# Performance work log

Hardware: AMD Instinct MI355X
Metric: run time of the kernel (lower is better)

## Reference

```python
import jax, jax.numpy as jnp
import numpy as np

N = 2_097_152   # total nodes
G = 8_192       # graphs in the batch
T = 1_000       # diffusion steps


def setup_inputs() -> dict:
    key = jax.random.key(0)
    k1, k2, k3, k4, k5 = jax.random.split(key, 5)
    x0 = jax.random.normal(k1, (N, 3), jnp.float32)
    x1 = jax.random.normal(k2, (N, 3), jnp.float32)
    noise = jax.random.normal(k3, (N, 3), jnp.float32)
    beta = jnp.linspace(1e-4, 0.02, T).astype(jnp.float32)
    batch = jnp.sort(jax.random.randint(k4, (N,), 0, G, jnp.int32))
    time = jax.random.randint(k5, (N,), 0, T, jnp.int32)
    return dict(x0=x0, x1=x1, noise=noise, beta=beta, batch=batch, time=time)


def reference(x0, x1, noise, beta, batch, time):
    # ---- schedule buffers (computed from beta exactly as in __init__) ----
    std_fwd = jnp.sqrt(jnp.cumsum(beta))                      # [T]
    std_bwd = jnp.sqrt(jnp.flip(jnp.cumsum(jnp.flip(beta))))  # [T]
    denom = std_bwd ** 2 + std_fwd ** 2
    mu_x0 = std_fwd ** 2 / denom   # coef1 with sigma1=std_bwd, sigma2=std_fwd
    mu_x1 = std_bwd ** 2 / denom
    std_sb = jnp.sqrt(std_bwd ** 2 * std_fwd ** 2 / denom)

    # extract(coef, time, dim)[batch] == coef[time][batch] (per-node gather)
    idx = time[batch]                                         # [N]
    x_t = (mu_x0[idx, None] * x0 + mu_x1[idx, None] * x1
           + std_sb[idx, None] * noise)                       # [N,3]

    # ---- fused unbatch + match_com + Kabsch align over all G graphs ----
    seg = lambda v: jax.ops.segment_sum(v, batch, num_segments=G,
                                        indices_are_sorted=True)
    cnt = jnp.maximum(seg(jnp.ones((N,), x0.dtype)), 1.0)[:, None]  # [G,1]
    com_x0 = seg(x0) / cnt                                    # [G,3]
    com_xt = seg(x_t) / cnt                                   # [G,3]
    x0c = x0 - com_x0[batch]   # match_com: shift x0 COM onto x_t COM
    xtc = x_t - com_xt[batch]

    # Kabsch: H_g = sum_i x0c_i xtc_i^T  -> rotation mapping x0 onto x_t
    H = seg(x0c[:, :, None] * xtc[:, None, :])                # [G,3,3]
    U, S, Vt = jnp.linalg.svd(H)
    d = jnp.sign(jnp.linalg.det(U) * jnp.linalg.det(Vt))      # [G]
    D = jnp.stack([jnp.ones_like(d), jnp.ones_like(d), d], axis=-1)  # [G,3]
    # R = V diag(1,1,d) U^T,  R_ij = Vt_ki D_k U_jk
    R = jnp.einsum('gki,gk,gjk->gij', Vt, D, U)               # [G,3,3]

    aligned_x0 = jnp.einsum('nij,nj->ni', R[batch], x0c) + com_xt[batch]

    target = (x_t - aligned_x0) / std_fwd[idx, None]
    return x_t, target
```

## Files before the change

kernel.cpp:

```cpp
#include <hip/hip_runtime.h>
#include <math.h>

#define GMAX 8192

__device__ float g_sched[4 * 1024];
__device__ int   g_starts[GMAX + 1];
__device__ float g_gparams[GMAX * 16];

__global__ __launch_bounds__(1024) void k_sched(const float* __restrict__ beta, int T) {
    __shared__ double sbeta[1024];
    __shared__ double buf[2][1024];
    int t = threadIdx.x;
    double b = (t < T) ? (double)beta[t] : 0.0;
    sbeta[t] = b;
    buf[0][t] = b;
    __syncthreads();
    int src = 0;
    for (int off = 1; off < 1024; off <<= 1) {
        double v = buf[src][t];
        if (t >= off) v += buf[src][t - off];
        buf[src ^ 1][t] = v;
        src ^= 1;
        __syncthreads();
    }
    double total = buf[src][T - 1];
    if (t < T) {
        double fwd2 = buf[src][t];
        double bwd2 = total - fwd2 + sbeta[t];
        double denom = fwd2 + bwd2;
        g_sched[t]          = (float)(fwd2 / denom);
        g_sched[1024 + t]   = (float)(bwd2 / denom);
        g_sched[2048 + t]   = (float)sqrt(fwd2 * bwd2 / denom);
        g_sched[3072 + t]   = (float)(1.0 / sqrt(fwd2));
    }
}

__global__ void k_starts(const int* __restrict__ batch, int N, int G) {
    int g = blockIdx.x * blockDim.x + threadIdx.x;
    if (g > G) return;
    int lo = 0, hi = N;
    while (lo < hi) {
        int mid = (lo + hi) >> 1;
        if (batch[mid] < g) lo = mid + 1; else hi = mid;
    }
    g_starts[g] = lo;
}

__device__ void kabsch_store(const float* sum, int n, float c0, float c1,
                             float cs, float isf, float* p) {
    double fn = (double)(n > 0 ? n : 1);
    double H[3][3];
    #pragma unroll
    for (int a = 0; a < 3; ++a)
        #pragma unroll
        for (int b = 0; b < 3; ++b)
            H[a][b] = (double)sum[6 + 3*a + b] - (double)sum[a] * (double)sum[3 + b] / fn;

    double A[3][3];
    #pragma unroll
    for (int i = 0; i < 3; ++i)
        #pragma unroll
        for (int j = 0; j < 3; ++j) {
            double acc = 0.0;
            #pragma unroll
            for (int k = 0; k < 3; ++k) acc += H[k][i] * H[k][j];
            A[i][j] = acc;
        }

    double V[3][3] = {{1,0,0},{0,1,0},{0,0,1}};
    for (int sweep = 0; sweep < 20; ++sweep) {
        double off = A[0][1]*A[0][1] + A[0][2]*A[0][2] + A[1][2]*A[1][2];
        double diag = A[0][0]*A[0][0] + A[1][1]*A[1][1] + A[2][2]*A[2][2];
        if (off <= 1e-28 * (diag + 1e-300)) break;
        for (int pi = 0; pi < 3; ++pi) {
            int P = (pi == 0) ? 0 : (pi == 1) ? 0 : 1;
            int Q = (pi == 0) ? 1 : (pi == 1) ? 2 : 2;
            double apq = A[P][Q];
            if (apq == 0.0) continue;
            double theta = (A[Q][Q] - A[P][P]) / (2.0 * apq);
            double tt = ((theta >= 0.0) ? 1.0 : -1.0) /
                        (fabs(theta) + sqrt(theta * theta + 1.0));
            double c = 1.0 / sqrt(tt * tt + 1.0);
            double s = tt * c;
            double app = A[P][P], aqq = A[Q][Q];
            A[P][P] = app - tt * apq;
            A[Q][Q] = aqq + tt * apq;
            A[P][Q] = A[Q][P] = 0.0;
            int Rr = 3 - P - Q;
            double arp = A[Rr][P], arq = A[Rr][Q];
            A[Rr][P] = A[P][Rr] = c * arp - s * arq;
            A[Rr][Q] = A[Q][Rr] = s * arp + c * arq;
            #pragma unroll
            for (int i = 0; i < 3; ++i) {
                double vip = V[i][P], viq = V[i][Q];
                V[i][P] = c * vip - s * viq;
                V[i][Q] = s * vip + c * viq;
            }
        }
    }
    double w[3] = {A[0][0], A[1][1], A[2][2]};
    int o0 = 0, o1 = 1, o2 = 2, tmp;
    if (w[o0] < w[o1]) { tmp = o0; o0 = o1; o1 = tmp; }
    if (w[o0] < w[o2]) { tmp = o0; o0 = o2; o2 = tmp; }
    if (w[o1] < w[o2]) { tmp = o1; o1 = o2; o2 = tmp; }

    double s0 = sqrt(fmax(w[o0], 0.0));
    double s1 = sqrt(fmax(w[o1], 0.0));
    double s2 = sqrt(fmax(w[o2], 0.0));
    double det = H[0][0]*(H[1][1]*H[2][2] - H[1][2]*H[2][1])
               - H[0][1]*(H[1][0]*H[2][2] - H[1][2]*H[2][0])
               + H[0][2]*(H[1][0]*H[2][1] - H[1][1]*H[2][0]);
    double d = (det >= 0.0) ? 1.0 : -1.0;
    double thr = 1e-9 * s0;
    double i0 = (s0 > 1e-300) ? 1.0 / s0 : 0.0;
    double i1 = (s1 > thr) ? 1.0 / s1 : 0.0;
    double i2 = (s2 > thr) ? d / s2 : 0.0;

    double B[3][3];
    #pragma unroll
    for (int i = 0; i < 3; ++i)
        #pragma unroll
        for (int j = 0; j < 3; ++j)
            B[i][j] = V[i][o0] * i0 * V[j][o0]
                    + V[i][o1] * i1 * V[j][o1]
                    + V[i][o2] * i2 * V[j][o2];

    double Rm[3][3];
    #pragma unroll
    for (int i = 0; i < 3; ++i)
        #pragma unroll
        for (int j = 0; j < 3; ++j)
            Rm[i][j] = B[i][0]*H[j][0] + B[i][1]*H[j][1] + B[i][2]*H[j][2];

    double com0[3], comt[3];
    #pragma unroll
    for (int a = 0; a < 3; ++a) { com0[a] = sum[a] / fn; comt[a] = sum[3+a] / fn; }

    #pragma unroll
    for (int i = 0; i < 3; ++i)
        #pragma unroll
        for (int j = 0; j < 3; ++j)
            p[3*i + j] = (float)Rm[i][j];
    #pragma unroll
    for (int i = 0; i < 3; ++i)
        p[9 + i] = (float)(comt[i] - (Rm[i][0]*com0[0] + Rm[i][1]*com0[1] + Rm[i][2]*com0[2]));
    p[12] = c0; p[13] = c1; p[14] = cs; p[15] = isf;
}

__global__ __launch_bounds__(256) void k_reduce(const float* __restrict__ x0,
                                               const float* __restrict__ x1,
                                               const float* __restrict__ noise,
                                               const int* __restrict__ tarr,
                                               float* __restrict__ out_xt) {
    int g = blockIdx.x;
    int s = g_starts[g], e = g_starts[g + 1];
    int tg = tarr[g];
    float c0 = g_sched[tg];
    float c1 = g_sched[1024 + tg];
    float cs = g_sched[2048 + tg];
    float isf = g_sched[3072 + tg];

    float acc[15];
    #pragma unroll
    for (int k = 0; k < 15; ++k) acc[k] = 0.0f;

    for (int i = s + (int)threadIdx.x; i < e; i += 256) {
        float a0 = x0[3*i], a1 = x0[3*i+1], a2 = x0[3*i+2];
        float b0 = x1[3*i], b1 = x1[3*i+1], b2 = x1[3*i+2];
        float n0 = noise[3*i], n1 = noise[3*i+1], n2 = noise[3*i+2];
        float t0 = c0*a0 + c1*b0 + cs*n0;
        float t1 = c0*a1 + c1*b1 + cs*n1;
        float t2 = c0*a2 + c1*b2 + cs*n2;
        out_xt[3*i] = t0; out_xt[3*i+1] = t1; out_xt[3*i+2] = t2;
        acc[0] += a0; acc[1] += a1; acc[2] += a2;
        acc[3] += t0; acc[4] += t1; acc[5] += t2;
        acc[6]  += a0*t0; acc[7]  += a0*t1; acc[8]  += a0*t2;
        acc[9]  += a1*t0; acc[10] += a1*t1; acc[11] += a1*t2;
        acc[12] += a2*t0; acc[13] += a2*t1; acc[14] += a2*t2;
    }

    #pragma unroll
    for (int k = 0; k < 15; ++k) {
        #pragma unroll
        for (int off = 32; off > 0; off >>= 1)
            acc[k] += __shfl_down(acc[k], off, 64);
    }
    __shared__ float red[4][15];
    int wid = threadIdx.x >> 6, lane = threadIdx.x & 63;
    if (lane == 0) {
        #pragma unroll
        for (int k = 0; k < 15; ++k) red[wid][k] = acc[k];
    }
    __syncthreads();
    if (threadIdx.x == 0) {
        float sum[15];
        #pragma unroll
        for (int k = 0; k < 15; ++k)
            sum[k] = red[0][k] + red[1][k] + red[2][k] + red[3][k];
        kabsch_store(sum, e - s, c0, c1, cs, isf, &g_gparams[g * 16]);
    }
}

__global__ __launch_bounds__(256) void k_final(const float* __restrict__ x0,
                                              const int* __restrict__ batch,
                                              const float* __restrict__ xt,
                                              float* __restrict__ out_tg,
                                              int N) {
    int i = blockIdx.x * 256 + (int)threadIdx.x;
    if (i >= N) return;
    int g = batch[i];
    const float* p = &g_gparams[g * 16];
    float a0 = x0[3*i], a1 = x0[3*i+1], a2 = x0[3*i+2];
    float t0 = xt[3*i], t1 = xt[3*i+1], t2 = xt[3*i+2];
    float al0 = p[0]*a0 + p[1]*a1 + p[2]*a2 + p[9];
    float al1 = p[3]*a0 + p[4]*a1 + p[5]*a2 + p[10];
    float al2 = p[6]*a0 + p[7]*a1 + p[8]*a2 + p[11];
    float isf = p[15];
    out_tg[3*i]   = (t0 - al0) * isf;
    out_tg[3*i+1] = (t1 - al1) * isf;
    out_tg[3*i+2] = (t2 - al2) * isf;
}

extern "C" void kernel_launch(void* const* d_in, const int* in_sizes, int n_in,
                              void* d_out, int out_size, void* d_ws, size_t ws_size,
                              hipStream_t stream) {
    const float* x0    = (const float*)d_in[0];
    const float* x1    = (const float*)d_in[1];
    const float* noise = (const float*)d_in[2];
    const float* beta  = (const float*)d_in[3];
    const int*   batch = (const int*)d_in[4];
    const int*   tarr  = (const int*)d_in[5];

    int N = in_sizes[4];
    int T = in_sizes[3];
    int G = GMAX;

    float* out_xt = (float*)d_out;
    float* out_tg = out_xt + (size_t)3 * N;

    k_sched<<<1, 1024, 0, stream>>>(beta, T);
    k_starts<<<(G + 1 + 255) / 256, 256, 0, stream>>>(batch, N, G);
    k_reduce<<<G, 256, 0, stream>>>(x0, x1, noise, tarr, out_xt);
    k_final<<<(N + 255) / 256, 256, 0, stream>>>(x0, batch, out_xt, out_tg, N);
}
```

Before: 196.7 us.

## Stage node data via float4 shared loads and split Kabsch into its own kernel

Merges the schedule and segment-start kernels into one launch. The reduce and final kernels now load x0, x1, noise and xt as float4 into shared memory per 256-node chunk, instead of doing strided scalar loads of 3-float records. The serial double-precision Kabsch solve, which ran on thread 0 at the end of every reduce block, moves to a separate kernel with one thread per graph, and per-graph sums pass through a global buffer. The final kernel runs one block per graph, so it no longer reads `batch`. The costs are an extra launch, extra `__syncthreads` per chunk, and idle lanes in partial chunks.

Measured after the change: 175.0 us. 1.12x faster.

```diff
diff --git a/kernel.cpp b/kernel.cpp
--- a/kernel.cpp
+++ b/kernel.cpp
@@ -5,45 +5,49 @@
 
 __device__ float g_sched[4 * 1024];
 __device__ int   g_starts[GMAX + 1];
+__device__ float g_sums[GMAX * 16];
 __device__ float g_gparams[GMAX * 16];
 
-__global__ __launch_bounds__(1024) void k_sched(const float* __restrict__ beta, int T) {
-    __shared__ double sbeta[1024];
-    __shared__ double buf[2][1024];
-    int t = threadIdx.x;
-    double b = (t < T) ? (double)beta[t] : 0.0;
-    sbeta[t] = b;
-    buf[0][t] = b;
-    __syncthreads();
-    int src = 0;
-    for (int off = 1; off < 1024; off <<= 1) {
-        double v = buf[src][t];
-        if (t >= off) v += buf[src][t - off];
-        buf[src ^ 1][t] = v;
-        src ^= 1;
-        __syncthreads();
-    }
-    double total = buf[src][T - 1];
-    if (t < T) {
-        double fwd2 = buf[src][t];
-        double bwd2 = total - fwd2 + sbeta[t];
-        double denom = fwd2 + bwd2;
-        g_sched[t]          = (float)(fwd2 / denom);
-        g_sched[1024 + t]   = (float)(bwd2 / denom);
-        g_sched[2048 + t]   = (float)sqrt(fwd2 * bwd2 / denom);
-        g_sched[3072 + t]   = (float)(1.0 / sqrt(fwd2));
-    }
-}
-
-__global__ void k_starts(const int* __restrict__ batch, int N, int G) {
-    int g = blockIdx.x * blockDim.x + threadIdx.x;
-    if (g > G) return;
-    int lo = 0, hi = N;
-    while (lo < hi) {
-        int mid = (lo + hi) >> 1;
-        if (batch[mid] < g) lo = mid + 1; else hi = mid;
-    }
-    g_starts[g] = lo;
+__global__ __launch_bounds__(1024) void k_prep(const float* __restrict__ beta,
+                                               const int* __restrict__ batch,
+                                               int T, int N, int G) {
+    if (blockIdx.x == 0) {
+        __shared__ double sbeta[1024];
+        __shared__ double buf[2][1024];
+        int t = threadIdx.x;
+        double b = (t < T) ? (double)beta[t] : 0.0;
+        sbeta[t] = b;
+        buf[0][t] = b;
+        __syncthreads();
+        int src = 0;
+        for (int off = 1; off < 1024; off <<= 1) {
+            double v = buf[src][t];
+            if (t >= off) v += buf[src][t - off];
+            buf[src ^ 1][t] = v;
+            src ^= 1;
+            __syncthreads();
+        }
+        double total = buf[src][T - 1];
+        if (t < T) {
+            double fwd2 = buf[src][t];
+            double bwd2 = total - fwd2 + sbeta[t];
+            double denom = fwd2 + bwd2;
+            g_sched[t]        = (float)(fwd2 / denom);
+            g_sched[1024 + t] = (float)(bwd2 / denom);
+            g_sched[2048 + t] = (float)sqrt(fwd2 * bwd2 / denom);
+            g_sched[3072 + t] = (float)(1.0 / sqrt(fwd2));
+        }
+    } else {
+        int g = (int)(blockIdx.x - 1) * 1024 + (int)threadIdx.x;
+        if (g <= G) {
+            int lo = 0, hi = N;
+            while (lo < hi) {
+                int mid = (lo + hi) >> 1;
+                if (batch[mid] < g) lo = mid + 1; else hi = mid;
+            }
+            g_starts[g] = lo;
+        }
+    }
 }
 
 __device__ void kabsch_store(const float* sum, int n, float c0, float c1,
@@ -82,9 +86,9 @@
                         (fabs(theta) + sqrt(theta * theta + 1.0));
             double c = 1.0 / sqrt(tt * tt + 1.0);
             double s = tt * c;
-            double app = A[P][P], aqq = A[Q][Q];
-            A[P][P] = app - tt * apq;
-            A[Q][Q] = aqq + tt * apq;
+            double apq2 = A[P][Q];
+            A[P][P] -= tt * apq2;
+            A[Q][Q] += tt * apq2;
             A[P][Q] = A[Q][P] = 0.0;
             int Rr = 3 - P - Q;
             double arp = A[Rr][P], arq = A[Rr][Q];
@@ -148,77 +152,139 @@
 }
 
 __global__ __launch_bounds__(256) void k_reduce(const float* __restrict__ x0,
-                                               const float* __restrict__ x1,
-                                               const float* __restrict__ noise,
-                                               const int* __restrict__ tarr,
-                                               float* __restrict__ out_xt) {
+                                                const float* __restrict__ x1,
+                                                const float* __restrict__ noise,
+                                                const int* __restrict__ tarr,
+                                                float* __restrict__ out_xt,
+                                                int total4) {
+    __shared__ __align__(16) float sA[776];
+    __shared__ __align__(16) float sB[776];
+    __shared__ __align__(16) float sN[776];
+    __shared__ float red[15][257];
+
     int g = blockIdx.x;
     int s = g_starts[g], e = g_starts[g + 1];
     int tg = tarr[g];
     float c0 = g_sched[tg];
     float c1 = g_sched[1024 + tg];
     float cs = g_sched[2048 + tg];
+
+    float acc[15];
+    #pragma unroll
+    for (int k = 0; k < 15; ++k) acc[k] = 0.0f;
+
+    const int tid = (int)threadIdx.x;
+
+    for (int cb = s; cb < e; cb += 256) {
+        int m = e - cb; if (m > 256) m = 256;
+        int fb = (3 * cb) & ~3;
+        int nf4 = ((3 * (cb + m)) - fb + 3) >> 2;
+        if (tid < nf4) {
+            int i4 = (fb >> 2) + tid;
+            if (i4 < total4) {
+                ((float4*)sA)[tid] = ((const float4*)x0)[i4];
+                ((float4*)sB)[tid] = ((const float4*)x1)[i4];
+                ((float4*)sN)[tid] = ((const float4*)noise)[i4];
+            }
+        }
+        __syncthreads();
+        if (tid < m) {
+            int off = 3 * (cb + tid) - fb;
+            float a0 = sA[off], a1 = sA[off+1], a2 = sA[off+2];
+            float b0 = sB[off], b1 = sB[off+1], b2 = sB[off+2];
+            float n0 = sN[off], n1 = sN[off+1], n2 = sN[off+2];
+            float t0 = c0*a0 + c1*b0 + cs*n0;
+            float t1 = c0*a1 + c1*b1 + cs*n1;
+            float t2 = c0*a2 + c1*b2 + cs*n2;
+            int oi = 3 * (cb + tid);
+            out_xt[oi] = t0; out_xt[oi+1] = t1; out_xt[oi+2] = t2;
+            acc[0] += a0; acc[1] += a1; acc[2] += a2;
+            acc[3] += t0; acc[4] += t1; acc[5] += t2;
+            acc[6]  += a0*t0; acc[7]  += a0*t1; acc[8]  += a0*t2;
+            acc[9]  += a1*t0; acc[10] += a1*t1; acc[11] += a1*t2;
+            acc[12] += a2*t0; acc[13] += a2*t1; acc[14] += a2*t2;
+        }
+        __syncthreads();
+    }
+
+    #pragma unroll
+    for (int v = 0; v < 15; ++v) red[v][tid] = acc[v];
+    __syncthreads();
+    int wv = tid >> 6;
+    int lane = tid & 63;
+    int v = wv * 4 + (lane >> 4);
+    int sub = lane & 15;
+    float x = 0.0f;
+    if (v < 15) {
+        #pragma unroll
+        for (int k = 0; k < 16; ++k) x += red[v][sub + (k << 4)];
+    }
+    x += __shfl_down(x, 8, 64);
+    x += __shfl_down(x, 4, 64);
+    x += __shfl_down(x, 2, 64);
+    x += __shfl_down(x, 1, 64);
+    if (v < 15 && sub == 0) g_sums[g * 16 + v] = x;
+}
+
+__global__ __launch_bounds__(256) void k_kabsch(const int* __restrict__ tarr) {
+    int g = blockIdx.x * 256 + (int)threadIdx.x;
+    if (g >= GMAX) return;
+    float sum[15];
+    #pragma unroll
+    for (int k = 0; k < 15; ++k) sum[k] = g_sums[g * 16 + k];
+    int n = g_starts[g + 1] - g_starts[g];
+    int tg = tarr[g];
+    float c0 = g_sched[tg];
+    float c1 = g_sched[1024 + tg];
+    float cs = g_sched[2048 + tg];
     float isf = g_sched[3072 + tg];
-
-    float acc[15];
-    #pragma unroll
-    for (int k = 0; k < 15; ++k) acc[k] = 0.0f;
-
-    for (int i = s + (int)threadIdx.x; i < e; i += 256) {
-        float a0 = x0[3*i], a1 = x0[3*i+1], a2 = x0[3*i+2];
-        float b0 = x1[3*i], b1 = x1[3*i+1], b2 = x1[3*i+2];
-        float n0 = noise[3*i], n1 = noise[3*i+1], n2 = noise[3*i+2];
-        float t0 = c0*a0 + c1*b0 + cs*n0;
-        float t1 = c0*a1 + c1*b1 + cs*n1;
-        float t2 = c0*a2 + c1*b2 + cs*n2;
-        out_xt[3*i] = t0; out_xt[3*i+1] = t1; out_xt[3*i+2] = t2;
-        acc[0] += a0; acc[1] += a1; acc[2] += a2;
-        acc[3] += t0; acc[4] += t1; acc[5] += t2;
-        acc[6]  += a0*t0; acc[7]  += a0*t1; acc[8]  += a0*t2;
-        acc[9]  += a1*t0; acc[10] += a1*t1; acc[11] += a1*t2;
-        acc[12] += a2*t0; acc[13] += a2*t1; acc[14] += a2*t2;
-    }
-
-    #pragma unroll
-    for (int k = 0; k < 15; ++k) {
-        #pragma unroll
-        for (int off = 32; off > 0; off >>= 1)
-            acc[k] += __shfl_down(acc[k], off, 64);
-    }
-    __shared__ float red[4][15];
-    int wid = threadIdx.x >> 6, lane = threadIdx.x & 63;
-    if (lane == 0) {
-        #pragma unroll
-        for (int k = 0; k < 15; ++k) red[wid][k] = acc[k];
-    }
-    __syncthreads();
-    if (threadIdx.x == 0) {
-        float sum[15];
-        #pragma unroll
-        for (int k = 0; k < 15; ++k)
-            sum[k] = red[0][k] + red[1][k] + red[2][k] + red[3][k];
-        kabsch_store(sum, e - s, c0, c1, cs, isf, &g_gparams[g * 16]);
-    }
+    kabsch_store(sum, n, c0, c1, cs, isf, &g_gparams[g * 16]);
 }
 
 __global__ __launch_bounds__(256) void k_final(const float* __restrict__ x0,
-                                              const int* __restrict__ batch,
-                                              const float* __restrict__ xt,
-                                              float* __restrict__ out_tg,
-                                              int N) {
-    int i = blockIdx.x * 256 + (int)threadIdx.x;
-    if (i >= N) return;
-    int g = batch[i];
+                                               const float* __restrict__ xt,
+                                               float* __restrict__ out_tg,
+                                               int total4) {
+    __shared__ __align__(16) float sA[776];
+    __shared__ __align__(16) float sT[776];
+    int g = blockIdx.x;
+    int s = g_starts[g], e = g_starts[g + 1];
+    if (s >= e) return;
+
     const float* p = &g_gparams[g * 16];
-    float a0 = x0[3*i], a1 = x0[3*i+1], a2 = x0[3*i+2];
-    float t0 = xt[3*i], t1 = xt[3*i+1], t2 = xt[3*i+2];
-    float al0 = p[0]*a0 + p[1]*a1 + p[2]*a2 + p[9];
-    float al1 = p[3]*a0 + p[4]*a1 + p[5]*a2 + p[10];
-    float al2 = p[6]*a0 + p[7]*a1 + p[8]*a2 + p[11];
+    float r00 = p[0], r01 = p[1], r02 = p[2];
+    float r10 = p[3], r11 = p[4], r12 = p[5];
+    float r20 = p[6], r21 = p[7], r22 = p[8];
+    float tv0 = p[9], tv1 = p[10], tv2 = p[11];
     float isf = p[15];
-    out_tg[3*i]   = (t0 - al0) * isf;
-    out_tg[3*i+1] = (t1 - al1) * isf;
-    out_tg[3*i+2] = (t2 - al2) * isf;
+
+    const int tid = (int)threadIdx.x;
+    for (int cb = s; cb < e; cb += 256) {
+        int m = e - cb; if (m > 256) m = 256;
+        int fb = (3 * cb) & ~3;
+        int nf4 = ((3 * (cb + m)) - fb + 3) >> 2;
+        if (tid < nf4) {
+            int i4 = (fb >> 2) + tid;
+            if (i4 < total4) {
+                ((float4*)sA)[tid] = ((const float4*)x0)[i4];
+                ((float4*)sT)[tid] = ((const float4*)xt)[i4];
+            }
+        }
+        __syncthreads();
+        if (tid < m) {
+            int off = 3 * (cb + tid) - fb;
+            float a0 = sA[off], a1 = sA[off+1], a2 = sA[off+2];
+            float w0 = sT[off], w1 = sT[off+1], w2 = sT[off+2];
+            float al0 = r00*a0 + r01*a1 + r02*a2 + tv0;
+            float al1 = r10*a0 + r11*a1 + r12*a2 + tv1;
+            float al2 = r20*a0 + r21*a1 + r22*a2 + tv2;
+            int oi = 3 * (cb + tid);
+            out_tg[oi]   = (w0 - al0) * isf;
+            out_tg[oi+1] = (w1 - al1) * isf;
+            out_tg[oi+2] = (w2 - al2) * isf;
+        }
+        __syncthreads();
+    }
 }
 
 extern "C" void kernel_launch(void* const* d_in, const int* in_sizes, int n_in,
@@ -234,12 +300,13 @@
     int N = in_sizes[4];
     int T = in_sizes[3];
     int G = GMAX;
+    int total4 = (3 * N) >> 2;
 
     float* out_xt = (float*)d_out;
     float* out_tg = out_xt + (size_t)3 * N;
 
-    k_sched<<<1, 1024, 0, stream>>>(beta, T);
-    k_starts<<<(G + 1 + 255) / 256, 256, 0, stream>>>(batch, N, G);
-    k_reduce<<<G, 256, 0, stream>>>(x0, x1, noise, tarr, out_xt);
-    k_final<<<(N + 255) / 256, 256, 0, stream>>>(x0, batch, out_xt, out_tg, N);
-}
+    k_prep<<<1 + (G + 1 + 1023) / 1024, 1024, 0, stream>>>(beta, batch, T, N, G);
+    k_reduce<<<G, 256, 0, stream>>>(x0, x1, noise, tarr, out_xt, total4);
+    k_kabsch<<<(G + 255) / 256, 256, 0, stream>>>(tarr);
+    k_final<<<G, 256, 0, stream>>>(x0, out_xt, out_tg, total4);
+}
```

## Replace per-graph reduction with flat node-parallel segmented reduction and atomics

Applied to the files above, without the earlier changes.

Per-graph blocks with binary-searched segment starts are replaced by a flat kernel in which each thread handles four nodes through float4 loads. Each wavefront does a segmented shuffle reduction and flushes per-graph sums, including the node count, to a global buffer with atomics. The Kabsch solve moves to its own one-thread-per-graph kernel, and the final pass is vectorised the same way. This targets the load imbalance and uncoalesced stride-3 accesses of the block-per-graph reduction, at the cost of atomic contention, float atomic nondeterminism, and the assumption that N is a multiple of 1024.

Result: faster. 168.3 us (-14.4%).

```diff
diff --git a/kernel.cpp b/kernel.cpp
--- a/kernel.cpp
+++ b/kernel.cpp
@@ -4,46 +4,117 @@
 #define GMAX 8192
 
 __device__ float g_sched[4 * 1024];
-__device__ int   g_starts[GMAX + 1];
+__device__ float g_sums[GMAX * 16];
 __device__ float g_gparams[GMAX * 16];
 
-__global__ __launch_bounds__(1024) void k_sched(const float* __restrict__ beta, int T) {
-    __shared__ double sbeta[1024];
-    __shared__ double buf[2][1024];
-    int t = threadIdx.x;
-    double b = (t < T) ? (double)beta[t] : 0.0;
-    sbeta[t] = b;
-    buf[0][t] = b;
-    __syncthreads();
-    int src = 0;
-    for (int off = 1; off < 1024; off <<= 1) {
-        double v = buf[src][t];
-        if (t >= off) v += buf[src][t - off];
-        buf[src ^ 1][t] = v;
-        src ^= 1;
+__global__ __launch_bounds__(1024) void k_prep(const float* __restrict__ beta, int T) {
+    if (blockIdx.x == 0) {
+        __shared__ double sbeta[1024];
+        __shared__ double buf[2][1024];
+        int t = threadIdx.x;
+        double b = (t < T) ? (double)beta[t] : 0.0;
+        sbeta[t] = b;
+        buf[0][t] = b;
         __syncthreads();
-    }
-    double total = buf[src][T - 1];
-    if (t < T) {
-        double fwd2 = buf[src][t];
-        double bwd2 = total - fwd2 + sbeta[t];
-        double denom = fwd2 + bwd2;
-        g_sched[t]          = (float)(fwd2 / denom);
-        g_sched[1024 + t]   = (float)(bwd2 / denom);
-        g_sched[2048 + t]   = (float)sqrt(fwd2 * bwd2 / denom);
-        g_sched[3072 + t]   = (float)(1.0 / sqrt(fwd2));
-    }
-}
-
-__global__ void k_starts(const int* __restrict__ batch, int N, int G) {
-    int g = blockIdx.x * blockDim.x + threadIdx.x;
-    if (g > G) return;
-    int lo = 0, hi = N;
-    while (lo < hi) {
-        int mid = (lo + hi) >> 1;
-        if (batch[mid] < g) lo = mid + 1; else hi = mid;
-    }
-    g_starts[g] = lo;
+        int src = 0;
+        for (int off = 1; off < 1024; off <<= 1) {
+            double v = buf[src][t];
+            if (t >= off) v += buf[src][t - off];
+            buf[src ^ 1][t] = v;
+            src ^= 1;
+            __syncthreads();
+        }
+        double total = buf[src][T - 1];
+        if (t < T) {
+            double fwd2 = buf[src][t];
+            double bwd2 = total - fwd2 + sbeta[t];
+            double denom = fwd2 + bwd2;
+            g_sched[t]        = (float)(fwd2 / denom);
+            g_sched[1024 + t] = (float)(bwd2 / denom);
+            g_sched[2048 + t] = (float)sqrt(fwd2 * bwd2 / denom);
+            g_sched[3072 + t] = (float)(1.0 / sqrt(fwd2));
+        }
+    } else {
+        int i = (int)(blockIdx.x - 1) * 1024 + (int)threadIdx.x;
+        ((float4*)g_sums)[i] = make_float4(0.f, 0.f, 0.f, 0.f);
+    }
+}
+
+__device__ inline void flush16(int g, const float* acc) {
+    float* dst = &g_sums[g * 16];
+    #pragma unroll
+    for (int k = 0; k < 16; ++k) atomicAdd(dst + k, acc[k]);
+}
+
+__global__ __launch_bounds__(256) void k_accum(const float* __restrict__ x0,
+                                               const float* __restrict__ x1,
+                                               const float* __restrict__ noise,
+                                               const int* __restrict__ batch,
+                                               const int* __restrict__ tarr,
+                                               float* __restrict__ out_xt) {
+    const int t = (int)blockIdx.x * 256 + (int)threadIdx.x;
+    const int4 gb = ((const int4*)batch)[t];
+    const int gs[4] = {gb.x, gb.y, gb.z, gb.w};
+
+    const float4* X0 = (const float4*)x0;
+    const float4* X1 = (const float4*)x1;
+    const float4* XN = (const float4*)noise;
+    float ax[12], bx[12], nx[12], tx[12];
+    #pragma unroll
+    for (int q = 0; q < 3; ++q) {
+        *(float4*)&ax[4*q] = X0[3*t + q];
+        *(float4*)&bx[4*q] = X1[3*t + q];
+        *(float4*)&nx[4*q] = XN[3*t + q];
+    }
+
+    float acc[16];
+    #pragma unroll
+    for (int k = 0; k < 16; ++k) acc[k] = 0.0f;
+
+    int gcur = gs[0];
+    int tg = tarr[gcur];
+    float c0 = g_sched[tg], c1 = g_sched[1024 + tg], cs = g_sched[2048 + tg];
+
+    #pragma unroll
+    for (int j = 0; j < 4; ++j) {
+        if (gs[j] != gcur) {
+            flush16(gcur, acc);
+            #pragma unroll
+            for (int k = 0; k < 16; ++k) acc[k] = 0.0f;
+            gcur = gs[j];
+            tg = tarr[gcur];
+            c0 = g_sched[tg]; c1 = g_sched[1024 + tg]; cs = g_sched[2048 + tg];
+        }
+        float a0 = ax[3*j], a1 = ax[3*j+1], a2 = ax[3*j+2];
+        float t0 = c0*a0 + c1*bx[3*j]   + cs*nx[3*j];
+        float t1 = c0*a1 + c1*bx[3*j+1] + cs*nx[3*j+1];
+        float t2 = c0*a2 + c1*bx[3*j+2] + cs*nx[3*j+2];
+        tx[3*j] = t0; tx[3*j+1] = t1; tx[3*j+2] = t2;
+        acc[0] += a0; acc[1] += a1; acc[2] += a2;
+        acc[3] += t0; acc[4] += t1; acc[5] += t2;
+        acc[6]  += a0*t0; acc[7]  += a0*t1; acc[8]  += a0*t2;
+        acc[9]  += a1*t0; acc[10] += a1*t1; acc[11] += a1*t2;
+        acc[12] += a2*t0; acc[13] += a2*t1; acc[14] += a2*t2;
+        acc[15] += 1.0f;
+    }
+
+    float4* OUT = (float4*)out_xt;
+    #pragma unroll
+    for (int q = 0; q < 3; ++q) OUT[3*t + q] = *(const float4*)&tx[4*q];
+
+    const int lane = (int)threadIdx.x & 63;
+    #pragma unroll
+    for (int off = 1; off < 64; off <<= 1) {
+        int gq = __shfl_down(gcur, off, 64);
+        bool valid = (lane + off < 64) && (gq == gcur);
+        #pragma unroll
+        for (int k = 0; k < 16; ++k) {
+            float xq = __shfl_down(acc[k], off, 64);
+            if (valid) acc[k] += xq;
+        }
+    }
+    int gprev = __shfl_up(gcur, 1, 64);
+    if (lane == 0 || gprev != gcur) flush16(gcur, acc);
 }
 
 __device__ void kabsch_store(const float* sum, int n, float c0, float c1,
@@ -82,9 +153,8 @@
                         (fabs(theta) + sqrt(theta * theta + 1.0));
             double c = 1.0 / sqrt(tt * tt + 1.0);
             double s = tt * c;
-            double app = A[P][P], aqq = A[Q][Q];
-            A[P][P] = app - tt * apq;
-            A[Q][Q] = aqq + tt * apq;
+            A[P][P] -= tt * apq;
+            A[Q][Q] += tt * apq;
             A[P][Q] = A[Q][P] = 0.0;
             int Rr = 3 - P - Q;
             double arp = A[Rr][P], arq = A[Rr][Q];
@@ -147,78 +217,66 @@
     p[12] = c0; p[13] = c1; p[14] = cs; p[15] = isf;
 }
 
-__global__ __launch_bounds__(256) void k_reduce(const float* __restrict__ x0,
-                                               const float* __restrict__ x1,
-                                               const float* __restrict__ noise,
-                                               const int* __restrict__ tarr,
-                                               float* __restrict__ out_xt) {
-    int g = blockIdx.x;
-    int s = g_starts[g], e = g_starts[g + 1];
+__global__ __launch_bounds__(256) void k_kabsch(const int* __restrict__ tarr) {
+    int g = (int)blockIdx.x * 256 + (int)threadIdx.x;
+    if (g >= GMAX) return;
+    float sum[16];
+    #pragma unroll
+    for (int q = 0; q < 4; ++q)
+        *(float4*)&sum[4*q] = ((const float4*)&g_sums[g * 16])[q];
+    int n = (int)(sum[15] + 0.5f);
     int tg = tarr[g];
     float c0 = g_sched[tg];
     float c1 = g_sched[1024 + tg];
     float cs = g_sched[2048 + tg];
     float isf = g_sched[3072 + tg];
-
-    float acc[15];
-    #pragma unroll
-    for (int k = 0; k < 15; ++k) acc[k] = 0.0f;
-
-    for (int i = s + (int)threadIdx.x; i < e; i += 256) {
-        float a0 = x0[3*i], a1 = x0[3*i+1], a2 = x0[3*i+2];
-        float b0 = x1[3*i], b1 = x1[3*i+1], b2 = x1[3*i+2];
-        float n0 = noise[3*i], n1 = noise[3*i+1], n2 = noise[3*i+2];
-        float t0 = c0*a0 + c1*b0 + cs*n0;
-        float t1 = c0*a1 + c1*b1 + cs*n1;
-        float t2 = c0*a2 + c1*b2 + cs*n2;
-        out_xt[3*i] = t0; out_xt[3*i+1] = t1; out_xt[3*i+2] = t2;
-        acc[0] += a0; acc[1] += a1; acc[2] += a2;
-        acc[3] += t0; acc[4] += t1; acc[5] += t2;
-        acc[6]  += a0*t0; acc[7]  += a0*t1; acc[8]  += a0*t2;
-        acc[9]  += a1*t0; acc[10] += a1*t1; acc[11] += a1*t2;
-        acc[12] += a2*t0; acc[13] += a2*t1; acc[14] += a2*t2;
-    }
-
-    #pragma unroll
-    for (int k = 0; k < 15; ++k) {
-        #pragma unroll
-        for (int off = 32; off > 0; off >>= 1)
-            acc[k] += __shfl_down(acc[k], off, 64);
-    }
-    __shared__ float red[4][15];
-    int wid = threadIdx.x >> 6, lane = threadIdx.x & 63;
-    if (lane == 0) {
-        #pragma unroll
-        for (int k = 0; k < 15; ++k) red[wid][k] = acc[k];
-    }
-    __syncthreads();
-    if (threadIdx.x == 0) {
-        float sum[15];
-        #pragma unroll
-        for (int k = 0; k < 15; ++k)
-            sum[k] = red[0][k] + red[1][k] + red[2][k] + red[3][k];
-        kabsch_store(sum, e - s, c0, c1, cs, isf, &g_gparams[g * 16]);
-    }
+    kabsch_store(sum, n, c0, c1, cs, isf, &g_gparams[g * 16]);
 }
 
 __global__ __launch_bounds__(256) void k_final(const float* __restrict__ x0,
-                                              const int* __restrict__ batch,
-                                              const float* __restrict__ xt,
-                                              float* __restrict__ out_tg,
-                                              int N) {
-    int i = blockIdx.x * 256 + (int)threadIdx.x;
-    if (i >= N) return;
-    int g = batch[i];
-    const float* p = &g_gparams[g * 16];
-    float a0 = x0[3*i], a1 = x0[3*i+1], a2 = x0[3*i+2];
-    float t0 = xt[3*i], t1 = xt[3*i+1], t2 = xt[3*i+2];
-    float al0 = p[0]*a0 + p[1]*a1 + p[2]*a2 + p[9];
-    float al1 = p[3]*a0 + p[4]*a1 + p[5]*a2 + p[10];
-    float al2 = p[6]*a0 + p[7]*a1 + p[8]*a2 + p[11];
-    float isf = p[15];
-    out_tg[3*i]   = (t0 - al0) * isf;
-    out_tg[3*i+1] = (t1 - al1) * isf;
-    out_tg[3*i+2] = (t2 - al2) * isf;
+                                               const float* __restrict__ xt,
+                                               const int* __restrict__ batch,
+                                               float* __restrict__ out_tg) {
+    const int t = (int)blockIdx.x * 256 + (int)threadIdx.x;
+    const int4 gb = ((const int4*)batch)[t];
+    const int gs[4] = {gb.x, gb.y, gb.z, gb.w};
+
+    const float4* XA = (const float4*)x0;
+    const float4* XT = (const float4*)xt;
+    float ax[12], wx[12], ox[12];
+    #pragma unroll
+    for (int q = 0; q < 3; ++q) {
+        *(float4*)&ax[4*q] = XA[3*t + q];
+        *(float4*)&wx[4*q] = XT[3*t + q];
+    }
+
+    int gcur = gs[0];
+    float pr[16];
+    #pragma unroll
+    for (int q = 0; q < 4; ++q)
+        *(float4*)&pr[4*q] = ((const float4*)&g_gparams[gcur * 16])[q];
+
+    #pragma unroll
+    for (int j = 0; j < 4; ++j) {
+        if (gs[j] != gcur) {
+            gcur = gs[j];
+            #pragma unroll
+            for (int q = 0; q < 4; ++q)
+                *(float4*)&pr[4*q] = ((const float4*)&g_gparams[gcur * 16])[q];
+        }
+        float a0 = ax[3*j], a1 = ax[3*j+1], a2 = ax[3*j+2];
+        float al0 = pr[0]*a0 + pr[1]*a1 + pr[2]*a2 + pr[9];
+        float al1 = pr[3]*a0 + pr[4]*a1 + pr[5]*a2 + pr[10];
+        float al2 = pr[6]*a0 + pr[7]*a1 + pr[8]*a2 + pr[11];
+        float isf = pr[15];
+        ox[3*j]   = (wx[3*j]   - al0) * isf;
+        ox[3*j+1] = (wx[3*j+1] - al1) * isf;
+        ox[3*j+2] = (wx[3*j+2] - al2) * isf;
+    }
+
+    float4* OUT = (float4*)out_tg;
+    #pragma unroll
+    for (int q = 0; q < 3; ++q) OUT[3*t + q] = *(const float4*)&ox[4*q];
 }
 
 extern "C" void kernel_launch(void* const* d_in, const int* in_sizes, int n_in,
@@ -233,13 +291,13 @@
 
     int N = in_sizes[4];
     int T = in_sizes[3];
-    int G = GMAX;
+    int nthreads = N / 4;
 
     float* out_xt = (float*)d_out;
     float* out_tg = out_xt + (size_t)3 * N;
 
-    k_sched<<<1, 1024, 0, stream>>>(beta, T);
-    k_starts<<<(G + 1 + 255) / 256, 256, 0, stream>>>(batch, N, G);
-    k_reduce<<<G, 256, 0, stream>>>(x0, x1, noise, tarr, out_xt);
-    k_final<<<(N + 255) / 256, 256, 0, stream>>>(x0, batch, out_xt, out_tg, N);
-}
+    k_prep<<<33, 1024, 0, stream>>>(beta, T);
+    k_accum<<<nthreads / 256, 256, 0, stream>>>(x0, x1, noise, batch, tarr, out_xt);
+    k_kabsch<<<GMAX / 256, 256, 0, stream>>>(tarr);
+    k_final<<<nthreads / 256, 256, 0, stream>>>(x0, out_xt, batch, out_tg);
+}
```
